# Optimization experiments

Measured on AMD Instinct MI355X. Metric: run time of the kernel, lower is better.

The kernel has to match this reference:

```python
import jax, jax.numpy as jnp
import numpy as np

B, S, D, H = 8, 1024, 2048, 16
DH = D // H  # 128


def setup_inputs() -> dict:
    key = jax.random.key(0)
    ks = jax.random.split(key, 6)
    sc = 1.0 / np.sqrt(D)
    return {
        "q": jax.random.normal(ks[0], (B, S, D), jnp.float32),
        "k": jax.random.normal(ks[1], (B, S, D), jnp.float32),
        "v": jax.random.normal(ks[2], (B, S, D), jnp.float32),
        "Wq": jax.random.normal(ks[3], (D, D), jnp.float32) * sc,
        "Wk": jax.random.normal(ks[4], (D, D), jnp.float32) * sc,
        "Wv": jax.random.normal(ks[5], (D, D), jnp.float32) * sc,
    }


def reference(q, k, v, Wq, Wk, Wv):
    # Linear projections (no bias), then split feature dim into H heads of DH.
    qh = (q @ Wq).reshape(B, S, H, DH)
    kh = (k @ Wk).reshape(B, S, H, DH)
    vh = (v @ Wv).reshape(B, S, H, DH)
    # scores: [B, H, Sq, Sk], scaled by sqrt(d_head)
    scores = jnp.einsum("bqhd,bkhd->bhqk", qh, kh) / jnp.sqrt(
        jnp.asarray(DH, qh.dtype)
    )
    probs = jax.nn.softmax(scores, axis=-1)
    out = jnp.einsum("bhqk,bkhd->bqhd", probs, vh).reshape(B, S, D)
    return out.astype(jnp.float32)
```

## Files before the change

### kernel.cpp

```cpp
#include <hip/hip_runtime.h>
#include <hip/hip_bf16.h>
#include <math.h>

#define BB 8
#define SS 1024
#define DD 2048
#define HH 16
#define DHD 128

typedef float  v4f  __attribute__((ext_vector_type(4)));
typedef short  v4s  __attribute__((ext_vector_type(4)));
typedef short  v8s  __attribute__((ext_vector_type(8)));
typedef __bf16 v8bf __attribute__((ext_vector_type(8)));

#define GLOBAL_AS __attribute__((address_space(1)))
#define LDS_AS    __attribute__((address_space(3)))

__device__ __forceinline__ unsigned short f2b(float f) {
    union { float f; unsigned int u; } x; x.f = f;
    unsigned int r = x.u + 0x7fffu + ((x.u >> 16) & 1u);
    return (unsigned short)(r >> 16);
}

__device__ __forceinline__ v8bf ldsv8(const unsigned short* p) {
    return __builtin_bit_cast(v8bf, *(const v8s*)p);
}

__global__ __launch_bounds__(256) void cvt_f32_bf16(const float* __restrict__ src,
                                                    unsigned short* __restrict__ dst,
                                                    int n4) {
    int i = blockIdx.x * blockDim.x + threadIdx.x;
    int stride = gridDim.x * blockDim.x;
    for (; i < n4; i += stride) {
        v4f f = ((const v4f*)src)[i];
        v4s o;
        o[0] = (short)f2b(f[0]); o[1] = (short)f2b(f[1]);
        o[2] = (short)f2b(f[2]); o[3] = (short)f2b(f[3]);
        ((v4s*)dst)[i] = o;
    }
}

__global__ __launch_bounds__(256) void wtrans_kernel(const float* __restrict__ W,
                                                     unsigned short* __restrict__ WT) {
    __shared__ float t[64][65];
    int nb = blockIdx.x * 64;
    int kb = blockIdx.y * 64;
    int tr = threadIdx.x >> 4;
    int tc = (threadIdx.x & 15) * 4;
#pragma unroll
    for (int i = 0; i < 4; i++) {
        int k = kb + tr + i * 16;
        v4f v = *(const v4f*)(W + (size_t)k * DD + nb + tc);
        t[tr + i * 16][tc + 0] = v[0];
        t[tr + i * 16][tc + 1] = v[1];
        t[tr + i * 16][tc + 2] = v[2];
        t[tr + i * 16][tc + 3] = v[3];
    }
    __syncthreads();
#pragma unroll
    for (int i = 0; i < 4; i++) {
        int n = nb + tr + i * 16;
        v4s o;
#pragma unroll
        for (int j = 0; j < 4; j++) o[j] = (short)f2b(t[tc + j][tr + i * 16]);
        *(v4s*)(WT + (size_t)n * DD + kb + tc) = o;
    }
}


#define STAGE_A(bb, gg, tt) do {                                              \
    __builtin_amdgcn_global_load_lds(                                         \
        (const GLOBAL_AS void*)(pA0 + (size_t)(gg) * 64 * K + (size_t)(tt) * 64), \
        (LDS_AS void*)(&sA[(bb) * 16384 + ldsA0 + (gg) * 4096]), 16, 0, 0);   \
    __builtin_amdgcn_global_load_lds(                                         \
        (const GLOBAL_AS void*)(pA1 + (size_t)(gg) * 64 * K + (size_t)(tt) * 64), \
        (LDS_AS void*)(&sA[(bb) * 16384 + ldsA1 + (gg) * 4096]), 16, 0, 0);   \
} while (0)

#define STAGE_B(bb, gg, tt) do {                                              \
    __builtin_amdgcn_global_load_lds(                                         \
        (const GLOBAL_AS void*)(pB0 + (size_t)(gg) * 32 * K + (size_t)(tt) * 64), \
        (LDS_AS void*)(&sB[(bb) * 16384 + ldsB0 + (gg) * 2048]), 16, 0, 0);   \
    __builtin_amdgcn_global_load_lds(                                         \
        (const GLOBAL_AS void*)(pB1 + (size_t)(gg) * 32 * K + (size_t)(tt) * 64), \
        (LDS_AS void*)(&sB[(bb) * 16384 + ldsB1 + (gg) * 2048]), 16, 0, 0);   \
} while (0)

#define PHASE(mh, nh, DOLDA, DOLDB, STAGE_STMT, WAIT_STMT) do {               \
    STAGE_STMT;                                                               \
    if (DOLDA) {                                                              \
        _Pragma("unroll")                                                     \
        for (int i = 0; i < 4; i++) {                                         \
            af[i][0] = ldsv8(sAb + aRow + (mh) * 4096 + i * 1024 + c0);       \
            af[i][1] = ldsv8(sAb + aRow + (mh) * 4096 + i * 1024 + c1);       \
        }                                                                     \
    }                                                                         \
    if (DOLDB) {                                                              \
        _Pragma("unroll")                                                     \
        for (int j = 0; j < 2; j++) {                                         \
            bf2[j][0] = ldsv8(sBb + bRow + (nh) * 2048 + j * 1024 + c0);      \
            bf2[j][1] = ldsv8(sBb + bRow + (nh) * 2048 + j * 1024 + c1);      \
        }                                                                     \
    }                                                                         \
    _Pragma("unroll")                                                         \
    for (int i = 0; i < 4; i++) {                                             \
        _Pragma("unroll")                                                     \
        for (int j = 0; j < 2; j++)                                           \
            acc[(mh) * 4 + i][(nh) * 2 + j] =                                 \
                __builtin_amdgcn_mfma_f32_16x16x32_bf16(                      \
                    af[i][0], bf2[j][0], acc[(mh) * 4 + i][(nh) * 2 + j], 0, 0, 0); \
    }                                                                         \
    _Pragma("unroll")                                                         \
    for (int i = 0; i < 4; i++) {                                             \
        _Pragma("unroll")                                                     \
        for (int j = 0; j < 2; j++)                                           \
            acc[(mh) * 4 + i][(nh) * 2 + j] =                                 \
                __builtin_amdgcn_mfma_f32_16x16x32_bf16(                      \
                    af[i][1], bf2[j][1], acc[(mh) * 4 + i][(nh) * 2 + j], 0, 0, 0); \
    }                                                                         \
    WAIT_STMT;                                                                \
    __builtin_amdgcn_s_barrier();                                             \
} while (0)

__global__ __launch_bounds__(512, 2) void gemm256(const unsigned short* __restrict__ A,
                                                  const unsigned short* __restrict__ BT,
                                                  unsigned short* __restrict__ C,
                                                  float scale, int vmode,
                                                  int M, int N, int K) {
    __shared__ __align__(16) unsigned short sA[2 * 16384];
    __shared__ __align__(16) unsigned short sB[2 * 16384];

    const int tid  = threadIdx.x;
    const int lane = tid & 63;
    const int w    = tid >> 6;
    const int qcol = lane & 15;
    const int quad = lane >> 4;
    const int l3   = lane >> 3;
    const int l7   = lane & 7;

    const int bid = blockIdx.x;
    const int bm  = ((bid & 7) * 4 + ((bid >> 3) & 3)) * 256;
    const int bn  = (bid >> 5) * 256;

    const int wm = (w >> 2) * 128;
    const int wn = (w & 3) * 64;

    const int gchunk = (l7 ^ l3) * 8;
    const int iA0 = w * 2, iA1 = w * 2 + 1;
    const int raA0 = (iA0 >> 3) * 128 + (iA0 & 7) * 8;
    const int raA1 = (iA1 >> 3) * 128 + (iA1 & 7) * 8;
    const int rbB0 = (iA0 >> 2) * 64 + (iA0 & 3) * 8;
    const int rbB1 = (iA1 >> 2) * 64 + (iA1 & 3) * 8;
    const unsigned short* pA0 = A  + (size_t)(bm + raA0 + l3) * K + gchunk;
    const unsigned short* pA1 = A  + (size_t)(bm + raA1 + l3) * K + gchunk;
    const unsigned short* pB0 = BT + (size_t)(bn + rbB0 + l3) * K + gchunk;
    const unsigned short* pB1 = BT + (size_t)(bn + rbB1 + l3) * K + gchunk;
    const int ldsA0 = raA0 * 64, ldsA1 = raA1 * 64;
    const int ldsB0 = rbB0 * 64, ldsB1 = rbB1 * 64;

    const int c0   = ((quad ^ l7) & 7) * 8;
    const int c1   = c0 ^ 32;
    const int aRow = (wm + qcol) * 64;
    const int bRow = (wn + qcol) * 64;

    v4f acc[8][4];
#pragma unroll
    for (int i = 0; i < 8; i++)
#pragma unroll
        for (int j = 0; j < 4; j++) acc[i][j] = (v4f){0.f, 0.f, 0.f, 0.f};

    v8bf af[4][2];
    v8bf bf2[2][2];

    const int nt = K >> 6;

    STAGE_A(0, 0, 0);
    STAGE_B(0, 0, 0);
    STAGE_B(0, 1, 0);
    STAGE_A(0, 1, 0);
    asm volatile("s_waitcnt vmcnt(4)");
    __builtin_amdgcn_s_barrier();

    for (int t = 0; t < nt - 1; ++t) {
        const int buf = t & 1, nbuf = buf ^ 1;
        const unsigned short* sAb = &sA[buf * 16384];
        const unsigned short* sBb = &sB[buf * 16384];

        PHASE(0, 0, 1, 1, STAGE_A(nbuf, 0, t + 1),
              asm volatile("s_waitcnt vmcnt(4)"));
        PHASE(0, 1, 0, 1, STAGE_B(nbuf, 0, t + 1),
              asm volatile("s_waitcnt vmcnt(4)"));
        PHASE(1, 1, 1, 0, STAGE_B(nbuf, 1, t + 1), );
        PHASE(1, 0, 0, 1, STAGE_A(nbuf, 1, t + 1),
              asm volatile("s_waitcnt vmcnt(4)"));
    }

    {
        const int buf = (nt - 1) & 1;
        const unsigned short* sAb = &sA[buf * 16384];
        const unsigned short* sBb = &sB[buf * 16384];
        PHASE(0, 0, 1, 1, , asm volatile("s_waitcnt vmcnt(2)"));
        PHASE(0, 1, 0, 1, , asm volatile("s_waitcnt vmcnt(0)"));
        PHASE(1, 1, 1, 0, , );
        PHASE(1, 0, 0, 1, , );
    }

    if (vmode == 0) {
#pragma unroll
        for (int mi = 0; mi < 8; mi++)
#pragma unroll
            for (int nj = 0; nj < 4; nj++)
#pragma unroll
                for (int r = 0; r < 4; r++) {
                    int row = bm + wm + mi * 16 + quad * 4 + r;
                    int col = bn + wn + nj * 16 + qcol;
                    C[(size_t)row * N + col] = f2b(acc[mi][nj][r] * scale);
                }
    } else {
#pragma unroll
        for (int mi = 0; mi < 8; mi++)
#pragma unroll
            for (int nj = 0; nj < 4; nj++)
#pragma unroll
                for (int r = 0; r < 4; r++) {
                    int row = bm + wm + mi * 16 + quad * 4 + r;
                    int col = bn + wn + nj * 16 + qcol;
                    size_t idx = ((size_t)(row >> 10) * 2048 + col) * 1024 + (row & 1023);
                    C[idx] = f2b(acc[mi][nj][r] * scale);
                }
    }
}

__global__ __launch_bounds__(256, 4) void attn_kernel(const unsigned short* __restrict__ qh,
                                                      const unsigned short* __restrict__ kh,
                                                      const unsigned short* __restrict__ vt,
                                                      float* __restrict__ out) {
    __shared__ __align__(16) unsigned short sK[64 * 128];
    __shared__ __align__(16) unsigned short sV[128 * 64];
    __shared__ __align__(16) unsigned short sP[4 * 16 * 64];

    int lane = threadIdx.x & 63, w = threadIdx.x >> 6;
    int b = blockIdx.z, h = blockIdx.y;
    int q0 = blockIdx.x * 64 + w * 16;
    int qcol = lane & 15, quad = lane >> 4;

    const unsigned short* qp = qh + (size_t)(b * SS + q0 + qcol) * DD + h * DHD;
    v8bf bq[4];
#pragma unroll
    for (int kk = 0; kk < 4; kk++)
        bq[kk] = __builtin_bit_cast(v8bf, *(const v8s*)(qp + kk * 32 + quad * 8));

    int ko[4];
#pragma unroll
    for (int j = 0; j < 4; j++) {
        int key = w * 16 + j * 4 + (lane >> 4);
        ko[j] = key * DD + (((lane & 15) ^ (key & 15)) * 8);
    }
    int vo0 = (w * 32 + (lane >> 3)) * SS + (((lane & 7) ^ (lane >> 3)) * 8);

    const unsigned short* kcur = kh + (size_t)b * SS * DD + h * DHD;
    const unsigned short* vcur = vt + (size_t)(b * HH + h) * DHD * SS;
    unsigned short* kl0 = &sK[(w * 16) * 128];
    unsigned short* vl0 = &sV[(w * 32) * 64];
    unsigned short* sPw = &sP[w * 1024];

    int pw[4], pr[2];
#pragma unroll
    for (int kf = 0; kf < 4; kf++)
        pw[kf] = qcol * 64 + (((kf * 2 + (quad >> 1)) ^ (qcol & 7)) * 8) + (quad & 1) * 4;
#pragma unroll
    for (int ks = 0; ks < 2; ks++)
        pr[ks] = qcol * 64 + (((ks * 4 + quad) ^ (qcol & 7)) * 8);

    float m_i = -1e30f, l_i = 0.f;
    v4f acc[8];
#pragma unroll
    for (int c = 0; c < 8; c++) acc[c] = (v4f){0.f, 0.f, 0.f, 0.f};

    for (int kb = 0; kb < SS; kb += 64) {
        __syncthreads();
#pragma unroll
        for (int j = 0; j < 4; j++)
            __builtin_amdgcn_global_load_lds((const GLOBAL_AS void*)(kcur + ko[j]),
                                             (LDS_AS void*)(kl0 + j * 4 * 128), 16, 0, 0);
#pragma unroll
        for (int j = 0; j < 4; j++)
            __builtin_amdgcn_global_load_lds((const GLOBAL_AS void*)(vcur + vo0 + j * 8 * SS),
                                             (LDS_AS void*)(vl0 + j * 8 * 64), 16, 0, 0);
        kcur += (size_t)64 * DD;
        vcur += 64;
        __syncthreads();

        v4f s[4];
#pragma unroll
        for (int kf = 0; kf < 4; kf++) {
            s[kf] = (v4f){0.f, 0.f, 0.f, 0.f};
#pragma unroll
            for (int kk = 0; kk < 4; kk++) {
                v8bf ak = __builtin_bit_cast(v8bf,
                    *(const v8s*)&sK[(kf * 16 + qcol) * 128 + (((kk * 4 + quad) ^ qcol) * 8)]);
                s[kf] = __builtin_amdgcn_mfma_f32_16x16x32_bf16(ak, bq[kk], s[kf], 0, 0, 0);
            }
        }

        float mx = -1e30f;
#pragma unroll
        for (int kf = 0; kf < 4; kf++)
#pragma unroll
            for (int r = 0; r < 4; r++) mx = fmaxf(mx, s[kf][r]);
        mx = fmaxf(mx, __shfl_xor(mx, 16));
        mx = fmaxf(mx, __shfl_xor(mx, 32));
        float m_new = fmaxf(m_i, mx);
        float rs = 0.f;
        v4s p[4];
#pragma unroll
        for (int kf = 0; kf < 4; kf++)
#pragma unroll
            for (int r = 0; r < 4; r++) {
                float pf = exp2f(s[kf][r] - m_new);
                rs += pf;
                p[kf][r] = (short)f2b(pf);
            }
        rs += __shfl_xor(rs, 16);
        rs += __shfl_xor(rs, 32);
        if (__any(mx > m_i)) {
            float alpha = exp2f(m_i - m_new);
            l_i *= alpha;
#pragma unroll
            for (int c = 0; c < 8; c++) {
                acc[c][0] *= alpha; acc[c][1] *= alpha;
                acc[c][2] *= alpha; acc[c][3] *= alpha;
            }
        }
        l_i += rs;
        m_i = m_new;

#pragma unroll
        for (int kf = 0; kf < 4; kf++)
            *(v4s*)&sPw[pw[kf]] = p[kf];

#pragma unroll
        for (int ks = 0; ks < 2; ks++) {
            v8bf pb = ldsv8(&sPw[pr[ks]]);
#pragma unroll
            for (int c = 0; c < 8; c++) {
                v8bf av = ldsv8(&sV[(c * 16 + qcol) * 64 + (((ks * 4 + quad) ^ (qcol & 7)) * 8)]);
                acc[c] = __builtin_amdgcn_mfma_f32_16x16x32_bf16(av, pb, acc[c], 0, 0, 0);
            }
        }
    }

    float rl = 1.0f / l_i;
    float* op = out + (size_t)(b * SS + q0 + qcol) * DD + h * DHD;
#pragma unroll
    for (int c = 0; c < 8; c++)
#pragma unroll
        for (int r = 0; r < 4; r++)
            op[c * 16 + quad * 4 + r] = acc[c][r] * rl;
}

extern "C" void kernel_launch(void* const* d_in, const int* in_sizes, int n_in,
                              void* d_out, int out_size, void* d_ws, size_t ws_size,
                              hipStream_t stream) {
    const float* ins[3]  = {(const float*)d_in[0], (const float*)d_in[1], (const float*)d_in[2]};
    const float* wins[3] = {(const float*)d_in[3], (const float*)d_in[4], (const float*)d_in[5]};
    char* ws = (char*)d_ws;
    unsigned short* abuf = (unsigned short*)(ws);
    unsigned short* wbuf = (unsigned short*)(ws + (size_t)32 * 1024 * 1024);
    unsigned short* qhb  = (unsigned short*)(ws + (size_t)40 * 1024 * 1024);
    unsigned short* khb  = (unsigned short*)(ws + (size_t)72 * 1024 * 1024);
    unsigned short* vtb  = (unsigned short*)(ws + (size_t)104 * 1024 * 1024);
    float* out = (float*)d_out;

    unsigned short* outs[3] = {qhb, khb, vtb};
    const float qscale = 0.12753139626246937f;
    float scales[3] = {qscale, 1.f, 1.f};
    int   vmodes[3] = {0, 0, 1};

    const int M = BB * SS, N = DD, K = DD;
    const int grid = (M / 256) * (N / 256);

    for (int i = 0; i < 3; i++) {
        cvt_f32_bf16<<<dim3(4096), dim3(256), 0, stream>>>(ins[i], abuf, (BB * SS * DD) / 4);
        wtrans_kernel<<<dim3(32, 32), dim3(256), 0, stream>>>(wins[i], wbuf);
        gemm256<<<dim3(grid), dim3(512), 0, stream>>>(abuf, wbuf, outs[i],
                                                      scales[i], vmodes[i], M, N, K);
    }
    attn_kernel<<<dim3(SS / 64, HH, BB), dim3(256), 0, stream>>>(qhb, khb, vtb, out);
}
```

Before: 584.3 us.

## Fuse fp32-to-bf16 activation conversion into GEMM and batch the three projections

Removes the separate activation conversion kernel. The GEMM now loads fp32 activations into registers, converts them to bf16 and writes them to LDS itself, while the weights still come in through direct global-to-LDS loads. The three weight transposes become one launch, and the three projection GEMMs become one launch with a grid dimension per projection. This cuts the fp32 read plus bf16 write-and-read round trip for 3×64MB of activations and several launches, at the cost of more register pressure, VGPR staging of A, and doubled global A bytes inside the GEMM.

```diff
diff --git a/kernel.cpp b/kernel.cpp
--- a/kernel.cpp
+++ b/kernel.cpp
@@ -16,32 +16,22 @@
 #define GLOBAL_AS __attribute__((address_space(1)))
 #define LDS_AS    __attribute__((address_space(3)))
 
-__device__ __forceinline__ unsigned short f2b(float f) {
-    union { float f; unsigned int u; } x; x.f = f;
-    unsigned int r = x.u + 0x7fffu + ((x.u >> 16) & 1u);
-    return (unsigned short)(r >> 16);
-}
-
 __device__ __forceinline__ v8bf ldsv8(const unsigned short* p) {
     return __builtin_bit_cast(v8bf, *(const v8s*)p);
 }
 
-__global__ __launch_bounds__(256) void cvt_f32_bf16(const float* __restrict__ src,
-                                                    unsigned short* __restrict__ dst,
-                                                    int n4) {
-    int i = blockIdx.x * blockDim.x + threadIdx.x;
-    int stride = gridDim.x * blockDim.x;
-    for (; i < n4; i += stride) {
-        v4f f = ((const v4f*)src)[i];
-        v4s o;
-        o[0] = (short)f2b(f[0]); o[1] = (short)f2b(f[1]);
-        o[2] = (short)f2b(f[2]); o[3] = (short)f2b(f[3]);
-        ((v4s*)dst)[i] = o;
-    }
-}
-
-__global__ __launch_bounds__(256) void wtrans_kernel(const float* __restrict__ W,
-                                                     unsigned short* __restrict__ WT) {
+__device__ __forceinline__ short bfb(float x) {
+    return __builtin_bit_cast(short, (__bf16)x);
+}
+
+__global__ __launch_bounds__(256) void wtrans_all(const float* __restrict__ W0,
+                                                  const float* __restrict__ W1,
+                                                  const float* __restrict__ W2,
+                                                  unsigned short* __restrict__ T0,
+                                                  unsigned short* __restrict__ T1,
+                                                  unsigned short* __restrict__ T2) {
+    const float* W = blockIdx.z == 0 ? W0 : (blockIdx.z == 1 ? W1 : W2);
+    unsigned short* WT = blockIdx.z == 0 ? T0 : (blockIdx.z == 1 ? T1 : T2);
     __shared__ float t[64][65];
     int nb = blockIdx.x * 64;
     int kb = blockIdx.y * 64;
@@ -62,46 +52,65 @@
         int n = nb + tr + i * 16;
         v4s o;
 #pragma unroll
-        for (int j = 0; j < 4; j++) o[j] = (short)f2b(t[tc + j][tr + i * 16]);
+        for (int j = 0; j < 4; j++) o[j] = bfb(t[tc + j][tr + i * 16]);
         *(v4s*)(WT + (size_t)n * DD + kb + tc) = o;
     }
 }
 
-
-#define STAGE_A(bb, gg, tt) do {                                              \
-    __builtin_amdgcn_global_load_lds(                                         \
-        (const GLOBAL_AS void*)(pA0 + (size_t)(gg) * 64 * K + (size_t)(tt) * 64), \
-        (LDS_AS void*)(&sA[(bb) * 16384 + ldsA0 + (gg) * 4096]), 16, 0, 0);   \
-    __builtin_amdgcn_global_load_lds(                                         \
-        (const GLOBAL_AS void*)(pA1 + (size_t)(gg) * 64 * K + (size_t)(tt) * 64), \
-        (LDS_AS void*)(&sA[(bb) * 16384 + ldsA1 + (gg) * 4096]), 16, 0, 0);   \
-} while (0)
 
 #define STAGE_B(bb, gg, tt) do {                                              \
     __builtin_amdgcn_global_load_lds(                                         \
-        (const GLOBAL_AS void*)(pB0 + (size_t)(gg) * 32 * K + (size_t)(tt) * 64), \
+        (const GLOBAL_AS void*)(pB0 + (size_t)(gg) * 32 * DD + (size_t)(tt) * 64), \
         (LDS_AS void*)(&sB[(bb) * 16384 + ldsB0 + (gg) * 2048]), 16, 0, 0);   \
     __builtin_amdgcn_global_load_lds(                                         \
-        (const GLOBAL_AS void*)(pB1 + (size_t)(gg) * 32 * K + (size_t)(tt) * 64), \
+        (const GLOBAL_AS void*)(pB1 + (size_t)(gg) * 32 * DD + (size_t)(tt) * 64), \
         (LDS_AS void*)(&sB[(bb) * 16384 + ldsB1 + (gg) * 2048]), 16, 0, 0);   \
 } while (0)
 
-#define PHASE(mh, nh, DOLDA, DOLDB, STAGE_STMT, WAIT_STMT) do {               \
-    STAGE_STMT;                                                               \
-    if (DOLDA) {                                                              \
-        _Pragma("unroll")                                                     \
-        for (int i = 0; i < 4; i++) {                                         \
-            af[i][0] = ldsv8(sAb + aRow + (mh) * 4096 + i * 1024 + c0);       \
-            af[i][1] = ldsv8(sAb + aRow + (mh) * 4096 + i * 1024 + c1);       \
-        }                                                                     \
+#define ALOAD(tt) do {                                                        \
+    ar[0][0][0] = *(const v4f*)(qA0 + (size_t)(tt) * 64);                     \
+    ar[0][0][1] = *(const v4f*)(qA0 + (size_t)(tt) * 64 + 4);                 \
+    ar[0][1][0] = *(const v4f*)(qA1 + (size_t)(tt) * 64);                     \
+    ar[0][1][1] = *(const v4f*)(qA1 + (size_t)(tt) * 64 + 4);                 \
+    ar[1][0][0] = *(const v4f*)(qA0 + (size_t)64 * DD + (size_t)(tt) * 64);   \
+    ar[1][0][1] = *(const v4f*)(qA0 + (size_t)64 * DD + (size_t)(tt) * 64 + 4); \
+    ar[1][1][0] = *(const v4f*)(qA1 + (size_t)64 * DD + (size_t)(tt) * 64);   \
+    ar[1][1][1] = *(const v4f*)(qA1 + (size_t)64 * DD + (size_t)(tt) * 64 + 4); \
+} while (0)
+
+#define PACK8(dst, va, vb) do {                                               \
+    v8s _o;                                                                   \
+    _o[0] = bfb((va)[0]); _o[1] = bfb((va)[1]);                               \
+    _o[2] = bfb((va)[2]); _o[3] = bfb((va)[3]);                               \
+    _o[4] = bfb((vb)[0]); _o[5] = bfb((vb)[1]);                               \
+    _o[6] = bfb((vb)[2]); _o[7] = bfb((vb)[3]);                               \
+    *(v8s*)(dst) = _o;                                                        \
+} while (0)
+
+#define AWRITE(bb, gg) do {                                                   \
+    PACK8(&sA[(bb) * 16384 + (raA0 + (gg) * 64 + l3) * 64 + l7 * 8],          \
+          ar[gg][0][0], ar[gg][0][1]);                                        \
+    PACK8(&sA[(bb) * 16384 + (raA1 + (gg) * 64 + l3) * 64 + l7 * 8],          \
+          ar[gg][1][0], ar[gg][1][1]);                                        \
+} while (0)
+
+#define LDA(mh) do {                                                          \
+    _Pragma("unroll")                                                         \
+    for (int i = 0; i < 4; i++) {                                             \
+        af[i][0] = ldsv8(sAb + aRow + (mh) * 4096 + i * 1024 + c0);           \
+        af[i][1] = ldsv8(sAb + aRow + (mh) * 4096 + i * 1024 + c1);           \
     }                                                                         \
-    if (DOLDB) {                                                              \
-        _Pragma("unroll")                                                     \
-        for (int j = 0; j < 2; j++) {                                         \
-            bf2[j][0] = ldsv8(sBb + bRow + (nh) * 2048 + j * 1024 + c0);      \
-            bf2[j][1] = ldsv8(sBb + bRow + (nh) * 2048 + j * 1024 + c1);      \
-        }                                                                     \
+} while (0)
+
+#define LDB(nh) do {                                                          \
+    _Pragma("unroll")                                                         \
+    for (int j = 0; j < 2; j++) {                                             \
+        bf2[j][0] = ldsv8(sBb + bRow + (nh) * 2048 + j * 1024 + c0);          \
+        bf2[j][1] = ldsv8(sBb + bRow + (nh) * 2048 + j * 1024 + c1);          \
     }                                                                         \
+} while (0)
+
+#define MMA(mh, nh) do {                                                      \
     _Pragma("unroll")                                                         \
     for (int i = 0; i < 4; i++) {                                             \
         _Pragma("unroll")                                                     \
@@ -118,17 +127,26 @@
                 __builtin_amdgcn_mfma_f32_16x16x32_bf16(                      \
                     af[i][1], bf2[j][1], acc[(mh) * 4 + i][(nh) * 2 + j], 0, 0, 0); \
     }                                                                         \
-    WAIT_STMT;                                                                \
-    __builtin_amdgcn_s_barrier();                                             \
-} while (0)
-
-__global__ __launch_bounds__(512, 2) void gemm256(const unsigned short* __restrict__ A,
-                                                  const unsigned short* __restrict__ BT,
-                                                  unsigned short* __restrict__ C,
-                                                  float scale, int vmode,
-                                                  int M, int N, int K) {
+} while (0)
+
+#define QSCALE 0.12753139626246937f
+
+__global__ __launch_bounds__(512, 2) void gemm_all(
+        const float* __restrict__ Aq, const float* __restrict__ Ak,
+        const float* __restrict__ Av,
+        const unsigned short* __restrict__ Bq, const unsigned short* __restrict__ Bk,
+        const unsigned short* __restrict__ Bv,
+        unsigned short* __restrict__ Cq, unsigned short* __restrict__ Ck,
+        unsigned short* __restrict__ Cv) {
     __shared__ __align__(16) unsigned short sA[2 * 16384];
     __shared__ __align__(16) unsigned short sB[2 * 16384];
+
+    const int proj = blockIdx.y;
+    const float* A; const unsigned short* BT; unsigned short* C;
+    float scale; int vmode;
+    if (proj == 0)      { A = Aq; BT = Bq; C = Cq; scale = QSCALE; vmode = 0; }
+    else if (proj == 1) { A = Ak; BT = Bk; C = Ck; scale = 1.f;    vmode = 0; }
+    else                { A = Av; BT = Bv; C = Cv; scale = 1.f;    vmode = 1; }
 
     const int tid  = threadIdx.x;
     const int lane = tid & 63;
@@ -151,11 +169,10 @@
     const int raA1 = (iA1 >> 3) * 128 + (iA1 & 7) * 8;
     const int rbB0 = (iA0 >> 2) * 64 + (iA0 & 3) * 8;
     const int rbB1 = (iA1 >> 2) * 64 + (iA1 & 3) * 8;
-    const unsigned short* pA0 = A  + (size_t)(bm + raA0 + l3) * K + gchunk;
-    const unsigned short* pA1 = A  + (size_t)(bm + raA1 + l3) * K + gchunk;
-    const unsigned short* pB0 = BT + (size_t)(bn + rbB0 + l3) * K + gchunk;
-    const unsigned short* pB1 = BT + (size_t)(bn + rbB1 + l3) * K + gchunk;
-    const int ldsA0 = raA0 * 64, ldsA1 = raA1 * 64;
+    const float* qA0 = A + (size_t)(bm + raA0 + l3) * DD + gchunk;
+    const float* qA1 = A + (size_t)(bm + raA1 + l3) * DD + gchunk;
+    const unsigned short* pB0 = BT + (size_t)(bn + rbB0 + l3) * DD + gchunk;
+    const unsigned short* pB1 = BT + (size_t)(bn + rbB1 + l3) * DD + gchunk;
     const int ldsB0 = rbB0 * 64, ldsB1 = rbB1 * 64;
 
     const int c0   = ((quad ^ l7) & 7) * 8;
@@ -171,14 +188,16 @@
 
     v8bf af[4][2];
     v8bf bf2[2][2];
-
-    const int nt = K >> 6;
-
-    STAGE_A(0, 0, 0);
+    v4f  ar[2][2][2];
+
+    const int nt = DD >> 6;
+
     STAGE_B(0, 0, 0);
     STAGE_B(0, 1, 0);
-    STAGE_A(0, 1, 0);
-    asm volatile("s_waitcnt vmcnt(4)");
+    ALOAD(0);
+    AWRITE(0, 0);
+    AWRITE(0, 1);
+    asm volatile("s_waitcnt vmcnt(0) lgkmcnt(0)");
     __builtin_amdgcn_s_barrier();
 
     for (int t = 0; t < nt - 1; ++t) {
@@ -186,23 +205,38 @@
         const unsigned short* sAb = &sA[buf * 16384];
         const unsigned short* sBb = &sB[buf * 16384];
 
-        PHASE(0, 0, 1, 1, STAGE_A(nbuf, 0, t + 1),
-              asm volatile("s_waitcnt vmcnt(4)"));
-        PHASE(0, 1, 0, 1, STAGE_B(nbuf, 0, t + 1),
-              asm volatile("s_waitcnt vmcnt(4)"));
-        PHASE(1, 1, 1, 0, STAGE_B(nbuf, 1, t + 1), );
-        PHASE(1, 0, 0, 1, STAGE_A(nbuf, 1, t + 1),
-              asm volatile("s_waitcnt vmcnt(4)"));
+        STAGE_B(nbuf, 0, t + 1);
+        STAGE_B(nbuf, 1, t + 1);
+        ALOAD(t + 1);
+        LDA(0); LDB(0);
+        MMA(0, 0);
+        __builtin_amdgcn_s_barrier();
+
+        LDB(1);
+        MMA(0, 1);
+        __builtin_amdgcn_s_barrier();
+
+        AWRITE(nbuf, 0);
+        AWRITE(nbuf, 1);
+        LDA(1);
+        MMA(1, 1);
+        asm volatile("s_waitcnt lgkmcnt(0)");
+        __builtin_amdgcn_s_barrier();
+
+        LDB(0);
+        MMA(1, 0);
+        asm volatile("s_waitcnt vmcnt(0)");
+        __builtin_amdgcn_s_barrier();
     }
 
     {
         const int buf = (nt - 1) & 1;
         const unsigned short* sAb = &sA[buf * 16384];
         const unsigned short* sBb = &sB[buf * 16384];
-        PHASE(0, 0, 1, 1, , asm volatile("s_waitcnt vmcnt(2)"));
-        PHASE(0, 1, 0, 1, , asm volatile("s_waitcnt vmcnt(0)"));
-        PHASE(1, 1, 1, 0, , );
-        PHASE(1, 0, 0, 1, , );
+        LDA(0); LDB(0); MMA(0, 0);
+        LDB(1);         MMA(0, 1);
+        LDA(1);         MMA(1, 1);
+        LDB(0);         MMA(1, 0);
     }
 
     if (vmode == 0) {
@@ -214,7 +248,7 @@
                 for (int r = 0; r < 4; r++) {
                     int row = bm + wm + mi * 16 + quad * 4 + r;
                     int col = bn + wn + nj * 16 + qcol;
-                    C[(size_t)row * N + col] = f2b(acc[mi][nj][r] * scale);
+                    C[(size_t)row * DD + col] = (unsigned short)bfb(acc[mi][nj][r] * scale);
                 }
     } else {
 #pragma unroll
@@ -226,7 +260,7 @@
                     int row = bm + wm + mi * 16 + quad * 4 + r;
                     int col = bn + wn + nj * 16 + qcol;
                     size_t idx = ((size_t)(row >> 10) * 2048 + col) * 1024 + (row & 1023);
-                    C[idx] = f2b(acc[mi][nj][r] * scale);
+                    C[idx] = (unsigned short)bfb(acc[mi][nj][r] * scale);
                 }
     }
 }
@@ -319,7 +353,7 @@
             for (int r = 0; r < 4; r++) {
                 float pf = exp2f(s[kf][r] - m_new);
                 rs += pf;
-                p[kf][r] = (short)f2b(pf);
+                p[kf][r] = bfb(pf);
             }
         rs += __shfl_xor(rs, 16);
         rs += __shfl_xor(rs, 32);
@@ -362,29 +396,22 @@
 extern "C" void kernel_launch(void* const* d_in, const int* in_sizes, int n_in,
                               void* d_out, int out_size, void* d_ws, size_t ws_size,
                               hipStream_t stream) {
-    const float* ins[3]  = {(const float*)d_in[0], (const float*)d_in[1], (const float*)d_in[2]};
-    const float* wins[3] = {(const float*)d_in[3], (const float*)d_in[4], (const float*)d_in[5]};
+    const float* q  = (const float*)d_in[0];
+    const float* k  = (const float*)d_in[1];
+    const float* v  = (const float*)d_in[2];
+    const float* Wq = (const float*)d_in[3];
+    const float* Wk = (const float*)d_in[4];
+    const float* Wv = (const float*)d_in[5];
     char* ws = (char*)d_ws;
-    unsigned short* abuf = (unsigned short*)(ws);
-    unsigned short* wbuf = (unsigned short*)(ws + (size_t)32 * 1024 * 1024);
-    unsigned short* qhb  = (unsigned short*)(ws + (size_t)40 * 1024 * 1024);
-    unsigned short* khb  = (unsigned short*)(ws + (size_t)72 * 1024 * 1024);
-    unsigned short* vtb  = (unsigned short*)(ws + (size_t)104 * 1024 * 1024);
+    unsigned short* wq  = (unsigned short*)(ws);
+    unsigned short* wk  = (unsigned short*)(ws + (size_t)8  * 1024 * 1024);
+    unsigned short* wv  = (unsigned short*)(ws + (size_t)16 * 1024 * 1024);
+    unsigned short* qhb = (unsigned short*)(ws + (size_t)24 * 1024 * 1024);
+    unsigned short* khb = (unsigned short*)(ws + (size_t)56 * 1024 * 1024);
+    unsigned short* vtb = (unsigned short*)(ws + (size_t)88 * 1024 * 1024);
     float* out = (float*)d_out;
 
-    unsigned short* outs[3] = {qhb, khb, vtb};
-    const float qscale = 0.12753139626246937f;
-    float scales[3] = {qscale, 1.f, 1.f};
-    int   vmodes[3] = {0, 0, 1};
-
-    const int M = BB * SS, N = DD, K = DD;
-    const int grid = (M / 256) * (N / 256);
-
-    for (int i = 0; i < 3; i++) {
-        cvt_f32_bf16<<<dim3(4096), dim3(256), 0, stream>>>(ins[i], abuf, (BB * SS * DD) / 4);
-        wtrans_kernel<<<dim3(32, 32), dim3(256), 0, stream>>>(wins[i], wbuf);
-        gemm256<<<dim3(grid), dim3(512), 0, stream>>>(abuf, wbuf, outs[i],
-                                                      scales[i], vmodes[i], M, N, K);
-    }
+    wtrans_all<<<dim3(32, 32, 3), dim3(256), 0, stream>>>(Wq, Wk, Wv, wq, wk, wv);
+    gemm_all<<<dim3(256, 3), dim3(512), 0, stream>>>(q, k, v, wq, wk, wv, qhb, khb, vtb);
     attn_kernel<<<dim3(SS / 64, HH, BB), dim3(256), 0, stream>>>(qhb, khb, vtb, out);
 }
```

Measured after the change: 585.1 us. No clear change (+0.1%).
